# Kernel tuning notes

Hardware: AMD Instinct MI355X
Metric: run time of the kernel (lower is better)

Reference implementation:

```python
import jax, jax.numpy as jnp
import numpy as np

DIM = 1024
HEADS = 16
DIM_HEAD = 64
INNER = HEADS * DIM_HEAD  # 1024
P = INNER  # num_param_tokens
B, N = 4, 2048
LN_EPS = 1e-5
NORM_EPS = 1e-12


def _pattention(x, key_tok, val_tok):
    # x: [..., dim_in]; key_tok: [P, dim_in]; val_tok: [P, dim_out]
    scale = key_tok.shape[1] ** (-0.5)
    sim = jnp.einsum('bnd,pd->bnp', x, key_tok) * scale
    # F.normalize(p=2, dim=-1) with eps=1e-12
    nrm = jnp.maximum(jnp.linalg.norm(sim, axis=-1, keepdims=True), NORM_EPS)
    attn = jax.nn.gelu(sim / nrm, approximate=False)  # torch F.gelu default = exact erf
    return jnp.einsum('bnp,pe->bne', attn, val_tok)


def setup_inputs() -> dict:
    key = jax.random.key(0)
    ks = jax.random.split(key, 11)
    d = {
        'x': jax.random.normal(ks[0], (B, N, DIM), dtype=jnp.float32),
        'ln_gamma': jnp.ones((DIM,), dtype=jnp.float32),
        'ln_beta': jnp.zeros((DIM,), dtype=jnp.float32),
        'q_key': jax.random.normal(ks[1], (P, DIM), dtype=jnp.float32),
        'q_val': jax.random.normal(ks[2], (P, INNER), dtype=jnp.float32),
        'k_key': jax.random.normal(ks[3], (P, DIM), dtype=jnp.float32),
        'k_val': jax.random.normal(ks[4], (P, INNER), dtype=jnp.float32),
        'v_key': jax.random.normal(ks[5], (P, DIM), dtype=jnp.float32),
        'v_val': jax.random.normal(ks[6], (P, INNER), dtype=jnp.float32),
        'o_key': jax.random.normal(ks[7], (P, INNER), dtype=jnp.float32),
        'o_val': jax.random.normal(ks[8], (P, DIM), dtype=jnp.float32),
    }
    return d


def reference(x, ln_gamma, ln_beta, q_key, q_val, k_key, k_val, v_key, v_val, o_key, o_val):
    # LayerNorm (torch default: elementwise affine, eps=1e-5)
    mu = jnp.mean(x, axis=-1, keepdims=True)
    var = jnp.mean(jnp.square(x - mu), axis=-1, keepdims=True)
    x_norm = (x - mu) / jnp.sqrt(var + LN_EPS) * ln_gamma + ln_beta

    q = _pattention(x_norm, q_key, q_val)  # [B, N, INNER]
    k = _pattention(x_norm, k_key, k_val)
    v = _pattention(x_norm, v_key, v_val)

    # b n (h d) -> b h n d
    def split_heads(t):
        return t.reshape(B, N, HEADS, DIM_HEAD).transpose(0, 2, 1, 3)

    q, k, v = split_heads(q), split_heads(k), split_heads(v)
    scale = DIM_HEAD ** (-0.5)
    dots = jnp.einsum('bhnd,bhmd->bhnm', q, k) * scale  # [B, H, N, N]
    attn = jax.nn.softmax(dots, axis=-1)  # dropout p=0 -> identity
    out = jnp.einsum('bhnm,bhmd->bhnd', attn, v)
    out = out.transpose(0, 2, 1, 3).reshape(B, N, INNER)  # b h n d -> b n (h d)
    return _pattention(out, o_key, o_val)
```

## Files before the change

### kernel.cpp

```cpp
#include <hip/hip_runtime.h>
#include <hip/hip_bf16.h>
#include <stdint.h>

#define DIMSZ 1024
#define BN_TOT 8192
#define NSEQ 2048
#define NHEADS 16
#define DHEAD 64

typedef __attribute__((ext_vector_type(8))) __bf16 bf16x8;
typedef __attribute__((ext_vector_type(4))) float f32x4;

__device__ __forceinline__ float bf2f(ushort u) {
  return __uint_as_float(((uint32_t)u) << 16);
}
__device__ __forceinline__ ushort f2bf(float f) {
  uint32_t u = __float_as_uint(f);
  u += 0x7FFFu + ((u >> 16) & 1u);
  return (ushort)(u >> 16);
}
__device__ __forceinline__ uint32_t cvt_pk_bf16(float lo, float hi) {
  uint32_t r;
  asm("v_cvt_pk_bf16_f32 %0, %1, %2" : "=v"(r) : "v"(lo), "v"(hi));
  return r;
}
__device__ __forceinline__ void gl_lds16(const ushort* g, ushort* l) {
  __builtin_amdgcn_global_load_lds(
      (const __attribute__((address_space(1))) void*)g,
      (__attribute__((address_space(3))) void*)l, 16, 0, 0);
}

__global__ __launch_bounds__(256) void layernorm_k(
    const float* __restrict__ x, const float* __restrict__ gamma,
    const float* __restrict__ beta, ushort* __restrict__ xn) {
  const int row = blockIdx.x;
  const int tid = threadIdx.x;
  const float* xr = x + (size_t)row * DIMSZ;
  float4 v = *(const float4*)(xr + tid * 4);
  float s = v.x + v.y + v.z + v.w;
  float ss = v.x * v.x + v.y * v.y + v.z * v.z + v.w * v.w;
#pragma unroll
  for (int o = 1; o < 64; o <<= 1) { s += __shfl_xor(s, o); ss += __shfl_xor(ss, o); }
  __shared__ float red[2][4];
  const int wid = tid >> 6;
  if ((tid & 63) == 0) { red[0][wid] = s; red[1][wid] = ss; }
  __syncthreads();
  s = red[0][0] + red[0][1] + red[0][2] + red[0][3];
  ss = red[1][0] + red[1][1] + red[1][2] + red[1][3];
  const float mu = s * (1.0f / DIMSZ);
  const float var = ss * (1.0f / DIMSZ) - mu * mu;
  const float rstd = rsqrtf(var + 1e-5f);
  float4 g = *(const float4*)(gamma + tid * 4);
  float4 bb = *(const float4*)(beta + tid * 4);
  ushort4 o4;
  o4.x = f2bf((v.x - mu) * rstd * g.x + bb.x);
  o4.y = f2bf((v.y - mu) * rstd * g.y + bb.y);
  o4.z = f2bf((v.z - mu) * rstd * g.z + bb.z);
  o4.w = f2bf((v.w - mu) * rstd * g.w + bb.w);
  *(ushort4*)(xn + (size_t)row * DIMSZ + tid * 4) = o4;
}

__global__ __launch_bounds__(256) void normgelu_bf_k(
    ushort* __restrict__ buf, const float* __restrict__ ssq) {
  const size_t row = (size_t)blockIdx.y * BN_TOT + blockIdx.x;
  ushort* p = buf + row * DIMSZ + threadIdx.x * 4;
  const float inv = 1.0f / fmaxf(sqrtf(ssq[row]), 1e-12f);
  ushort4 v = *(const ushort4*)p;
  ushort4 o4;
  float x0;
  x0 = bf2f(v.x) * inv; o4.x = f2bf(0.5f * x0 * (1.0f + erff(x0 * 0.70710678118654752f)));
  x0 = bf2f(v.y) * inv; o4.y = f2bf(0.5f * x0 * (1.0f + erff(x0 * 0.70710678118654752f)));
  x0 = bf2f(v.z) * inv; o4.z = f2bf(0.5f * x0 * (1.0f + erff(x0 * 0.70710678118654752f)));
  x0 = bf2f(v.w) * inv; o4.w = f2bf(0.5f * x0 * (1.0f + erff(x0 * 0.70710678118654752f)));
  *(ushort4*)p = o4;
}

__global__ void cvt4_k(const float* __restrict__ s0, const float* __restrict__ s1,
                       const float* __restrict__ s2, const float* __restrict__ s3,
                       ushort* __restrict__ out) {
  const int z = blockIdx.z;
  const float* in = (z == 0) ? s0 : (z == 1) ? s1 : (z == 2) ? s2 : s3;
  const int i = (blockIdx.x * 256 + threadIdx.x) * 4;
  float4 v = *(const float4*)(in + i);
  ushort4 o;
  o.x = f2bf(v.x); o.y = f2bf(v.y); o.z = f2bf(v.z); o.w = f2bf(v.w);
  *(ushort4*)(out + (size_t)z * DIMSZ * DIMSZ + i) = o;
}

__global__ __launch_bounds__(256) void transpose_cvt4_k(
    const float* __restrict__ s0, const float* __restrict__ s1,
    const float* __restrict__ s2, const float* __restrict__ s3,
    ushort* __restrict__ out) {
  __shared__ float t[32][33];
  const int z = blockIdx.z;
  const float* in = (z == 0) ? s0 : (z == 1) ? s1 : (z == 2) ? s2 : s3;
  ushort* dst = out + (size_t)z * DIMSZ * DIMSZ;
  const int tx = threadIdx.x & 31;
  const int ty = threadIdx.x >> 5;
  const int bx = blockIdx.x * 32;
  const int by = blockIdx.y * 32;
#pragma unroll
  for (int i = 0; i < 32; i += 8)
    t[ty + i][tx] = in[(size_t)(by + ty + i) * DIMSZ + bx + tx];
  __syncthreads();
#pragma unroll
  for (int i = 0; i < 32; i += 8)
    dst[(size_t)(bx + ty + i) * DIMSZ + by + tx] = f2bf(t[tx][ty + i]);
}

__global__ __launch_bounds__(256) void transpose_v_k(
    const ushort* __restrict__ vb, ushort* __restrict__ vt) {
  __shared__ ushort t[32][33];
  const int bh = blockIdx.x;
  const int nt = blockIdx.y;
  const int dt = blockIdx.z;
  const int b = bh >> 4, h = bh & 15;
  const int tx = threadIdx.x & 31;
  const int ty = threadIdx.x >> 5;
  const size_t inbase = ((size_t)b * NSEQ + nt * 32) * DIMSZ + h * DHEAD + dt * 32;
#pragma unroll
  for (int i = 0; i < 32; i += 8)
    t[ty + i][tx] = vb[inbase + (size_t)(ty + i) * DIMSZ + tx];
  __syncthreads();
  const size_t outbase = ((size_t)bh * DHEAD + dt * 32) * NSEQ + nt * 32;
#pragma unroll
  for (int i = 0; i < 32; i += 8)
    vt[outbase + (size_t)(ty + i) * NSEQ + tx] = t[tx][ty + i];
}

template <int OUT_BF16, int WRITE_SSQ, int A_PER_Z>
__global__ __launch_bounds__(256) void gemm_nt_k(
    const ushort* __restrict__ A, const ushort* __restrict__ B,
    void* __restrict__ C0, void* __restrict__ C1, void* __restrict__ C2,
    float* __restrict__ ssq, int M, int N, int K) {
  __shared__ ushort As[3][128 * 32];
  __shared__ ushort Bs[3][128 * 32];
  const int z = blockIdx.z;
  const ushort* Az = A + (A_PER_Z ? (size_t)z * M * K : 0);
  const ushort* Bz = B + (size_t)z * N * K;
  void* Cout = (z == 0) ? C0 : (z == 1) ? C1 : C2;
  float* sz = WRITE_SSQ ? (ssq + (size_t)z * M) : nullptr;
  const int tid = threadIdx.x;
  const int lane = tid & 63;
  const int wid = tid >> 6;
  const int i0 = blockIdx.x * 128;
  const int n0 = blockIdx.y * 128;
  const int wr = (wid >> 1) * 64;
  const int wc = (wid & 1) * 64;
  f32x4 acc[4][4];
#pragma unroll
  for (int m = 0; m < 4; ++m)
#pragma unroll
    for (int n = 0; n < 4; ++n) acc[m][n] = (f32x4){0.f, 0.f, 0.f, 0.f};
  const int fr = lane & 15;
  const int g = lane >> 4;
  const int kg = (g ^ ((fr >> 1) & 3)) * 8;
  const int srow = wid * 32 + (lane >> 2);
  const int skc = ((lane & 3) ^ ((lane >> 3) & 3)) * 8;
  const ushort* Ag = Az + (size_t)(i0 + srow) * K + skc;
  const ushort* Bg = Bz + (size_t)(n0 + srow) * K + skc;
  const int wb = wid * 1024;

#define STAGE_TILE(tt, bb)                                      \
  do {                                                          \
    gl_lds16(Ag + (tt) * 32, &As[bb][wb]);                      \
    gl_lds16(Ag + (size_t)16 * K + (tt) * 32, &As[bb][wb + 512]); \
    gl_lds16(Bg + (tt) * 32, &Bs[bb][wb]);                      \
    gl_lds16(Bg + (size_t)16 * K + (tt) * 32, &Bs[bb][wb + 512]); \
  } while (0)

  const int nt = K >> 5;
  STAGE_TILE(0, 0);
  STAGE_TILE(1, 1);
  asm volatile("s_waitcnt vmcnt(4)" ::: "memory");
  __builtin_amdgcn_s_barrier();

  int cur = 0;
  for (int t = 0; t < nt; ++t) {
    if (t + 2 < nt) {
      const int nb = (cur >= 1) ? cur - 1 : cur + 2;
      STAGE_TILE(t + 2, nb);
    }
    bf16x8 af[4], bfr[4];
#pragma unroll
    for (int m = 0; m < 4; ++m)
      af[m] = *(const bf16x8*)&As[cur][(wr + m * 16 + fr) * 32 + kg];
#pragma unroll
    for (int n = 0; n < 4; ++n)
      bfr[n] = *(const bf16x8*)&Bs[cur][(wc + n * 16 + fr) * 32 + kg];
#pragma unroll
    for (int m = 0; m < 4; ++m)
#pragma unroll
      for (int n = 0; n < 4; ++n)
        acc[m][n] = __builtin_amdgcn_mfma_f32_16x16x32_bf16(af[m], bfr[n], acc[m][n], 0, 0, 0);
    if (t + 2 < nt)
      asm volatile("s_waitcnt vmcnt(4)" ::: "memory");
    else
      asm volatile("s_waitcnt vmcnt(0)" ::: "memory");
    __builtin_amdgcn_s_barrier();
    cur = (cur == 2) ? 0 : cur + 1;
  }
#undef STAGE_TILE

  const int rq = lane >> 4;
#pragma unroll
  for (int m = 0; m < 4; ++m) {
#pragma unroll
    for (int n = 0; n < 4; ++n) {
#pragma unroll
      for (int rr = 0; rr < 4; ++rr) {
        const int row = i0 + wr + m * 16 + rq * 4 + rr;
        const int col = n0 + wc + n * 16 + fr;
        if (OUT_BF16)
          ((ushort*)Cout)[(size_t)row * N + col] = f2bf(acc[m][n][rr]);
        else
          ((float*)Cout)[(size_t)row * N + col] = acc[m][n][rr];
      }
    }
  }
  if (WRITE_SSQ) {
#pragma unroll
    for (int m = 0; m < 4; ++m) {
#pragma unroll
      for (int rr = 0; rr < 4; ++rr) {
        float s2 = acc[m][0][rr] * acc[m][0][rr] + acc[m][1][rr] * acc[m][1][rr] +
                   acc[m][2][rr] * acc[m][2][rr] + acc[m][3][rr] * acc[m][3][rr];
#pragma unroll
        for (int o = 1; o < 16; o <<= 1) s2 += __shfl_xor(s2, o);
        if (fr == 0) atomicAdd(&sz[i0 + wr + m * 16 + rq * 4 + rr], s2);
      }
    }
  }
}

__global__ __launch_bounds__(256, 3) void flash_mfma_k(
    const ushort* __restrict__ Qm, const ushort* __restrict__ Km,
    const ushort* __restrict__ Vt, ushort* __restrict__ Om) {
  __shared__ ushort Ks[64 * 72];
  __shared__ ushort Vs[65 * 72];
  __shared__ ushort Ps[4][32 * 72];
  const int tid = threadIdx.x;
  const int lane = tid & 63;
  const int wid = tid >> 6;
  const int bh = blockIdx.x;
  const int qb = blockIdx.y;
  const int bidx = bh >> 4;
  const int h = bh & 15;
  const size_t rowbase = (size_t)bidx * NSEQ;
  const int colbase = h * DHEAD;
  const int fr = lane & 15;
  const int g = lane >> 4;
  const int kg = g * 8;
  const int q0 = qb * 128 + wid * 32;

  if (tid < 64) Vs[64 * 72 + tid] = 0x3F80;

  bf16x8 qf[2][2];
#pragma unroll
  for (int m = 0; m < 2; ++m)
#pragma unroll
    for (int ks = 0; ks < 2; ++ks)
      qf[m][ks] = *(const bf16x8*)(Qm + (rowbase + q0 + m * 16 + fr) * (size_t)DIMSZ +
                                   colbase + ks * 32 + kg);

  f32x4 oaccT[2][4];
  f32x4 lacc[2];
#pragma unroll
  for (int m = 0; m < 2; ++m) {
#pragma unroll
    for (int n = 0; n < 4; ++n) oaccT[m][n] = (f32x4){0.f, 0.f, 0.f, 0.f};
    lacc[m] = (f32x4){0.f, 0.f, 0.f, 0.f};
  }
  float m2[2] = {-1e30f, -1e30f};
  const float c1 = 0.125f * 1.44269504088896340736f;

  const ushort* Kg = Km + rowbase * DIMSZ + colbase;
  const ushort* Vg = Vt + (size_t)bh * DHEAD * NSEQ;
  const int sr = tid >> 3;
  const int c8 = (tid & 7) * 8;

  uint4 k0 = *(const uint4*)(Kg + (size_t)sr * DIMSZ + c8);
  uint4 k1 = *(const uint4*)(Kg + (size_t)(sr + 32) * DIMSZ + c8);
  uint4 v0 = *(const uint4*)(Vg + (size_t)sr * NSEQ + c8);
  uint4 v1 = *(const uint4*)(Vg + (size_t)(sr + 32) * NSEQ + c8);

  for (int kt = 0; kt < NSEQ / 64; ++kt) {
    __syncthreads();
    *(uint4*)&Ks[sr * 72 + c8] = k0;
    *(uint4*)&Ks[(sr + 32) * 72 + c8] = k1;
    *(uint4*)&Vs[sr * 72 + c8] = v0;
    *(uint4*)&Vs[(sr + 32) * 72 + c8] = v1;
    __syncthreads();
    if (kt + 1 < NSEQ / 64) {
      k0 = *(const uint4*)(Kg + (size_t)((kt + 1) * 64 + sr) * DIMSZ + c8);
      k1 = *(const uint4*)(Kg + (size_t)((kt + 1) * 64 + sr + 32) * DIMSZ + c8);
      v0 = *(const uint4*)(Vg + (size_t)sr * NSEQ + (kt + 1) * 64 + c8);
      v1 = *(const uint4*)(Vg + (size_t)(sr + 32) * NSEQ + (kt + 1) * 64 + c8);
    }

#pragma unroll
    for (int m = 0; m < 2; ++m) {
      f32x4 s[4];
#pragma unroll
      for (int n = 0; n < 4; ++n) s[n] = (f32x4){0.f, 0.f, 0.f, 0.f};
      __builtin_amdgcn_s_setprio(1);
#pragma unroll
      for (int ks = 0; ks < 2; ++ks) {
        bf16x8 ak[4];
#pragma unroll
        for (int n = 0; n < 4; ++n)
          ak[n] = *(const bf16x8*)&Ks[(n * 16 + fr) * 72 + ks * 32 + kg];
#pragma unroll
        for (int n = 0; n < 4; ++n)
          s[n] = __builtin_amdgcn_mfma_f32_16x16x32_bf16(ak[n], qf[m][ks], s[n], 0, 0, 0);
      }
      __builtin_amdgcn_s_setprio(0);

      const float a0 = fmaxf(fmaxf(s[0][0], s[0][1]), s[0][2]);
      const float a1 = fmaxf(fmaxf(s[0][3], s[1][0]), s[1][1]);
      const float a2 = fmaxf(fmaxf(s[1][2], s[1][3]), s[2][0]);
      const float a3 = fmaxf(fmaxf(s[2][1], s[2][2]), s[2][3]);
      const float a4 = fmaxf(fmaxf(s[3][0], s[3][1]), s[3][2]);
      const float b0 = fmaxf(fmaxf(a0, a1), a2);
      const float b1 = fmaxf(fmaxf(a3, a4), s[3][3]);
      float tm = fmaxf(b0, b1);
      tm = fmaxf(tm, __shfl_xor(tm, 16));
      tm = fmaxf(tm, __shfl_xor(tm, 32));
      const float tm2 = tm * c1;
      if (!__all(tm2 <= m2[m] + 8.0f)) {
        const float mn2 = fmaxf(m2[m], tm2);
        const float al = exp2f(m2[m] - mn2);
        m2[m] = mn2;
        lacc[m] *= al;
#pragma unroll
        for (int n = 0; n < 4; ++n) oaccT[m][n] *= al;
      }
      const float mref = m2[m];
#pragma unroll
      for (int n = 0; n < 4; ++n)
#pragma unroll
        for (int rr = 0; rr < 4; ++rr)
          s[n][rr] = exp2f(fmaf(s[n][rr], c1, -mref));

      ushort* pw = &Ps[wid][0];
#pragma unroll
      for (int n = 0; n < 4; ++n) {
        uint2 w;
        w.x = cvt_pk_bf16(s[n][0], s[n][1]);
        w.y = cvt_pk_bf16(s[n][2], s[n][3]);
        *(uint2*)&pw[(m * 16 + fr) * 72 + n * 16 + g * 4] = w;
      }
    }

    __builtin_amdgcn_s_setprio(1);
#pragma unroll
    for (int ks = 0; ks < 2; ++ks) {
      bf16x8 av[4], pb[2];
      const bf16x8 av1 = *(const bf16x8*)&Vs[64 * 72 + ks * 32 + kg];
#pragma unroll
      for (int nd = 0; nd < 4; ++nd)
        av[nd] = *(const bf16x8*)&Vs[(nd * 16 + fr) * 72 + ks * 32 + kg];
#pragma unroll
      for (int m = 0; m < 2; ++m)
        pb[m] = *(const bf16x8*)&Ps[wid][(m * 16 + fr) * 72 + ks * 32 + kg];
#pragma unroll
      for (int m = 0; m < 2; ++m) {
#pragma unroll
        for (int nd = 0; nd < 4; ++nd)
          oaccT[m][nd] = __builtin_amdgcn_mfma_f32_16x16x32_bf16(av[nd], pb[m], oaccT[m][nd], 0, 0, 0);
        lacc[m] = __builtin_amdgcn_mfma_f32_16x16x32_bf16(av1, pb[m], lacc[m], 0, 0, 0);
      }
    }
    __builtin_amdgcn_s_setprio(0);
  }

#pragma unroll
  for (int m = 0; m < 2; ++m) {
    const float invl = 1.0f / lacc[m][0];
    const size_t row = rowbase + q0 + m * 16 + fr;
#pragma unroll
    for (int nd = 0; nd < 4; ++nd) {
      uint2 w;
      w.x = cvt_pk_bf16(oaccT[m][nd][0] * invl, oaccT[m][nd][1] * invl);
      w.y = cvt_pk_bf16(oaccT[m][nd][2] * invl, oaccT[m][nd][3] * invl);
      *(uint2*)(Om + row * DIMSZ + colbase + nd * 16 + g * 4) = w;
    }
  }
}

extern "C" void kernel_launch(void* const* d_in, const int* in_sizes, int n_in,
                              void* d_out, int out_size, void* d_ws, size_t ws_size,
                              hipStream_t stream) {
  (void)in_sizes; (void)n_in; (void)out_size; (void)ws_size;
  const float* x     = (const float*)d_in[0];
  const float* ln_g  = (const float*)d_in[1];
  const float* ln_b  = (const float*)d_in[2];
  const float* q_key = (const float*)d_in[3];
  const float* q_val = (const float*)d_in[4];
  const float* k_key = (const float*)d_in[5];
  const float* k_val = (const float*)d_in[6];
  const float* v_key = (const float*)d_in[7];
  const float* v_val = (const float*)d_in[8];
  const float* o_key = (const float*)d_in[9];
  const float* o_val = (const float*)d_in[10];
  float* out = (float*)d_out;

  char* ws = (char*)d_ws;
  const size_t MB = 1024 * 1024;
  ushort* xn    = (ushort*)(ws + 0 * MB);
  ushort* wkey  = (ushort*)(ws + 16 * MB);
  ushort* wvalT = (ushort*)(ws + 24 * MB);
  ushort* bufA  = (ushort*)(ws + 32 * MB);
  ushort* bufB  = (ushort*)(ws + 48 * MB);
  ushort* bufC  = (ushort*)(ws + 64 * MB);
  ushort* bufD  = (ushort*)(ws + 80 * MB);
  ushort* bufE  = (ushort*)(ws + 96 * MB);
  ushort* vscr  = (ushort*)d_out;
  float*  ssqb  = (float*)((char*)d_out + 24 * MB);

  const int NW = DIMSZ * DIMSZ;

  hipMemsetAsync(ssqb, 0, 4 * BN_TOT * sizeof(float), stream);
  layernorm_k<<<BN_TOT, 256, 0, stream>>>(x, ln_g, ln_b, xn);
  cvt4_k<<<dim3(1024, 1, 4), 256, 0, stream>>>(q_key, k_key, v_key, o_key, wkey);
  transpose_cvt4_k<<<dim3(32, 32, 4), 256, 0, stream>>>(q_val, k_val, v_val, o_val, wvalT);

  dim3 gg3(BN_TOT / 128, DIMSZ / 128, 3);
  dim3 gg1(BN_TOT / 128, DIMSZ / 128, 1);
  gemm_nt_k<1, 1, 0><<<gg3, 256, 0, stream>>>(
      xn, wkey, bufB, bufC, bufD, ssqb, BN_TOT, DIMSZ, DIMSZ);
  normgelu_bf_k<<<dim3(BN_TOT, 3), 256, 0, stream>>>(bufB, ssqb);
  gemm_nt_k<1, 0, 1><<<gg3, 256, 0, stream>>>(
      bufB, wvalT, bufA, bufE, vscr, nullptr, BN_TOT, DIMSZ, DIMSZ);

  transpose_v_k<<<dim3(64, 64, 2), 256, 0, stream>>>(vscr, bufD);
  flash_mfma_k<<<dim3(64, 16), 256, 0, stream>>>(bufA, bufE, bufD, bufB);

  gemm_nt_k<1, 1, 0><<<gg1, 256, 0, stream>>>(
      bufB, wkey + 3 * (size_t)NW, bufC, bufC, bufC, ssqb + 3 * BN_TOT,
      BN_TOT, DIMSZ, DIMSZ);
  normgelu_bf_k<<<dim3(BN_TOT, 1), 256, 0, stream>>>(bufC, ssqb + 3 * BN_TOT);
  gemm_nt_k<0, 0, 0><<<gg1, 256, 0, stream>>>(
      bufC, wvalT + 3 * (size_t)NW, out, out, out, nullptr, BN_TOT, DIMSZ, DIMSZ);
}
```

Baseline: 385.8 us.

## Double-buffer K/V shared tiles and defer cross-lane max reduction to rescale path

Turns the flash attention K/V LDS tiles into double buffers. The next tile is written to the alternate buffer while the current one is used, which cuts the two barriers per iteration down to one. The running-max shuffle reduction now runs only when a rescale is triggered, so the common path skips two cross-lane shuffles. The cost is more LDS per block, which could limit occupancy at 3 blocks per CU.

```diff
diff --git a/kernel.cpp b/kernel.cpp
--- a/kernel.cpp
+++ b/kernel.cpp
@@ -236,8 +236,8 @@
 __global__ __launch_bounds__(256, 3) void flash_mfma_k(
     const ushort* __restrict__ Qm, const ushort* __restrict__ Km,
     const ushort* __restrict__ Vt, ushort* __restrict__ Om) {
-  __shared__ ushort Ks[64 * 72];
-  __shared__ ushort Vs[65 * 72];
+  __shared__ ushort Ks[2][64 * 72];
+  __shared__ ushort Vs[2][65 * 72];
   __shared__ ushort Ps[4][32 * 72];
   const int tid = threadIdx.x;
   const int lane = tid & 63;
@@ -253,7 +253,10 @@
   const int kg = g * 8;
   const int q0 = qb * 128 + wid * 32;
 
-  if (tid < 64) Vs[64 * 72 + tid] = 0x3F80;
+  if (tid < 64) {
+    Vs[0][64 * 72 + tid] = 0x3F80;
+    Vs[1][64 * 72 + tid] = 0x3F80;
+  }
 
   bf16x8 qf[2][2];
 #pragma unroll
@@ -278,24 +281,37 @@
   const ushort* Vg = Vt + (size_t)bh * DHEAD * NSEQ;
   const int sr = tid >> 3;
   const int c8 = (tid & 7) * 8;
-
-  uint4 k0 = *(const uint4*)(Kg + (size_t)sr * DIMSZ + c8);
-  uint4 k1 = *(const uint4*)(Kg + (size_t)(sr + 32) * DIMSZ + c8);
-  uint4 v0 = *(const uint4*)(Vg + (size_t)sr * NSEQ + c8);
-  uint4 v1 = *(const uint4*)(Vg + (size_t)(sr + 32) * NSEQ + c8);
-
-  for (int kt = 0; kt < NSEQ / 64; ++kt) {
-    __syncthreads();
-    *(uint4*)&Ks[sr * 72 + c8] = k0;
-    *(uint4*)&Ks[(sr + 32) * 72 + c8] = k1;
-    *(uint4*)&Vs[sr * 72 + c8] = v0;
-    *(uint4*)&Vs[(sr + 32) * 72 + c8] = v1;
-    __syncthreads();
-    if (kt + 1 < NSEQ / 64) {
-      k0 = *(const uint4*)(Kg + (size_t)((kt + 1) * 64 + sr) * DIMSZ + c8);
-      k1 = *(const uint4*)(Kg + (size_t)((kt + 1) * 64 + sr + 32) * DIMSZ + c8);
-      v0 = *(const uint4*)(Vg + (size_t)sr * NSEQ + (kt + 1) * 64 + c8);
-      v1 = *(const uint4*)(Vg + (size_t)(sr + 32) * NSEQ + (kt + 1) * 64 + c8);
+  const int NT = NSEQ / 64;
+
+  {
+    uint4 a = *(const uint4*)(Kg + (size_t)sr * DIMSZ + c8);
+    uint4 b = *(const uint4*)(Kg + (size_t)(sr + 32) * DIMSZ + c8);
+    uint4 c = *(const uint4*)(Vg + (size_t)sr * NSEQ + c8);
+    uint4 d = *(const uint4*)(Vg + (size_t)(sr + 32) * NSEQ + c8);
+    *(uint4*)&Ks[0][sr * 72 + c8] = a;
+    *(uint4*)&Ks[0][(sr + 32) * 72 + c8] = b;
+    *(uint4*)&Vs[0][sr * 72 + c8] = c;
+    *(uint4*)&Vs[0][(sr + 32) * 72 + c8] = d;
+  }
+  uint4 k0 = *(const uint4*)(Kg + (size_t)(64 + sr) * DIMSZ + c8);
+  uint4 k1 = *(const uint4*)(Kg + (size_t)(64 + sr + 32) * DIMSZ + c8);
+  uint4 v0 = *(const uint4*)(Vg + (size_t)sr * NSEQ + 64 + c8);
+  uint4 v1 = *(const uint4*)(Vg + (size_t)(sr + 32) * NSEQ + 64 + c8);
+  __syncthreads();
+
+  for (int kt = 0; kt < NT; ++kt) {
+    const int cb = kt & 1;
+    if (kt + 1 < NT) {
+      *(uint4*)&Ks[cb ^ 1][sr * 72 + c8] = k0;
+      *(uint4*)&Ks[cb ^ 1][(sr + 32) * 72 + c8] = k1;
+      *(uint4*)&Vs[cb ^ 1][sr * 72 + c8] = v0;
+      *(uint4*)&Vs[cb ^ 1][(sr + 32) * 72 + c8] = v1;
+    }
+    if (kt + 2 < NT) {
+      k0 = *(const uint4*)(Kg + (size_t)((kt + 2) * 64 + sr) * DIMSZ + c8);
+      k1 = *(const uint4*)(Kg + (size_t)((kt + 2) * 64 + sr + 32) * DIMSZ + c8);
+      v0 = *(const uint4*)(Vg + (size_t)sr * NSEQ + (kt + 2) * 64 + c8);
+      v1 = *(const uint4*)(Vg + (size_t)(sr + 32) * NSEQ + (kt + 2) * 64 + c8);
     }
 
 #pragma unroll
@@ -309,7 +325,7 @@
         bf16x8 ak[4];
 #pragma unroll
         for (int n = 0; n < 4; ++n)
-          ak[n] = *(const bf16x8*)&Ks[(n * 16 + fr) * 72 + ks * 32 + kg];
+          ak[n] = *(const bf16x8*)&Ks[cb][(n * 16 + fr) * 72 + ks * 32 + kg];
 #pragma unroll
         for (int n = 0; n < 4; ++n)
           s[n] = __builtin_amdgcn_mfma_f32_16x16x32_bf16(ak[n], qf[m][ks], s[n], 0, 0, 0);
@@ -323,12 +339,12 @@
       const float a4 = fmaxf(fmaxf(s[3][0], s[3][1]), s[3][2]);
       const float b0 = fmaxf(fmaxf(a0, a1), a2);
       const float b1 = fmaxf(fmaxf(a3, a4), s[3][3]);
-      float tm = fmaxf(b0, b1);
-      tm = fmaxf(tm, __shfl_xor(tm, 16));
-      tm = fmaxf(tm, __shfl_xor(tm, 32));
-      const float tm2 = tm * c1;
+      const float tm2 = fmaxf(b0, b1) * c1;
       if (!__all(tm2 <= m2[m] + 8.0f)) {
-        const float mn2 = fmaxf(m2[m], tm2);
+        float gm = tm2;
+        gm = fmaxf(gm, __shfl_xor(gm, 16));
+        gm = fmaxf(gm, __shfl_xor(gm, 32));
+        const float mn2 = fmaxf(m2[m], gm);
         const float al = exp2f(m2[m] - mn2);
         m2[m] = mn2;
         lacc[m] *= al;
@@ -356,10 +372,10 @@
 #pragma unroll
     for (int ks = 0; ks < 2; ++ks) {
       bf16x8 av[4], pb[2];
-      const bf16x8 av1 = *(const bf16x8*)&Vs[64 * 72 + ks * 32 + kg];
+      const bf16x8 av1 = *(const bf16x8*)&Vs[cb][64 * 72 + ks * 32 + kg];
 #pragma unroll
       for (int nd = 0; nd < 4; ++nd)
-        av[nd] = *(const bf16x8*)&Vs[(nd * 16 + fr) * 72 + ks * 32 + kg];
+        av[nd] = *(const bf16x8*)&Vs[cb][(nd * 16 + fr) * 72 + ks * 32 + kg];
 #pragma unroll
       for (int m = 0; m < 2; ++m)
         pb[m] = *(const bf16x8*)&Ps[wid][(m * 16 + fr) * 72 + ks * 32 + kg];
@@ -372,6 +388,8 @@
       }
     }
     __builtin_amdgcn_s_setprio(0);
+
+    __syncthreads();
   }
 
 #pragma unroll
```

New measurement: 388.0 us. About the same (+0.6%).
